# Optimization experiments

Hardware: AMD Instinct MI355X
Metric: run time of the kernel (lower is better)

## Reference

```python
import jax, jax.numpy as jnp
import numpy as np

N = 100_000      # nodes
E = 1_600_000    # edges
EL = 200_000     # labeled edge pairs
NODE_DIM, HID = 32, 256
H2, H4 = HID // 2, HID // 4  # 128, 64


def _lin(k, fan_in, fan_out):
    kw, kb = jax.random.split(k)
    bound = 1.0 / np.sqrt(fan_in)
    W = jax.random.uniform(kw, (fan_in, fan_out), jnp.float32, -bound, bound)
    b = jax.random.uniform(kb, (fan_out,), jnp.float32, -bound, bound)
    return W, b


def setup_inputs() -> dict:
    key = jax.random.key(0)
    ks = jax.random.split(key, 12)
    x = jax.random.normal(ks[0], (N, NODE_DIM), jnp.float32)
    edge_index = jax.random.randint(ks[1], (2, E), 0, N, jnp.int64)
    edge_label_index = jax.random.randint(ks[2], (2, EL), 0, N, jnp.int64)
    enc_w1, enc_b1 = _lin(ks[3], NODE_DIM, HID)
    enc_w2, enc_b2 = _lin(ks[4], HID, H2)
    conv_w0, conv_b0 = _lin(ks[5], H2, H4)
    conv_w1, conv_b1 = _lin(ks[6], H4, H4)
    conv_w2, conv_b2 = _lin(ks[7], H4, H4)
    ep_w1, ep_b1 = _lin(ks[8], 2 * H4, H2)
    ep_w2, ep_b2 = _lin(ks[9], H2, H4)
    ep_w3, ep_b3 = _lin(ks[10], H4, 1)
    return dict(x=x, edge_index=edge_index, edge_label_index=edge_label_index,
                enc_w1=enc_w1, enc_b1=enc_b1, enc_w2=enc_w2, enc_b2=enc_b2,
                conv_w0=conv_w0, conv_b0=conv_b0, conv_w1=conv_w1, conv_b1=conv_b1,
                conv_w2=conv_w2, conv_b2=conv_b2,
                ep_w1=ep_w1, ep_b1=ep_b1, ep_w2=ep_w2, ep_b2=ep_b2, ep_w3=ep_w3, ep_b3=ep_b3)


def reference(x, edge_index, edge_label_index,
              enc_w1, enc_b1, enc_w2, enc_b2,
              conv_w0, conv_b0, conv_w1, conv_b1, conv_w2, conv_b2,
              ep_w1, ep_b1, ep_w2, ep_b2, ep_w3, ep_b3):
    # node encoder (dropout = identity in eval)
    h = jax.nn.relu(x @ enc_w1 + enc_b1)
    h = jax.nn.relu(h @ enc_w2 + enc_b2)           # [N, 128]

    # GCN normalization with self-loops (PyG gcn_norm, edge_weight=1)
    loops = jnp.arange(N, dtype=edge_index.dtype)
    src = jnp.concatenate([edge_index[0], loops])   # [E+N]
    dst = jnp.concatenate([edge_index[1], loops])
    deg = jax.ops.segment_sum(jnp.ones(E + N, jnp.float32), dst, num_segments=N)
    dinv = jnp.where(deg > 0, jax.lax.rsqrt(jnp.maximum(deg, 1.0)), 0.0)
    norm = (dinv[src] * dinv[dst])[:, None]          # [E+N, 1]

    def gcn(h, W, b):
        xw = h @ W                                   # transform first (PyG)
        agg = jax.ops.segment_sum(xw[src] * norm, dst, num_segments=N)
        return agg + b

    for W, b in ((conv_w0, conv_b0), (conv_w1, conv_b1), (conv_w2, conv_b2)):
        h_new = jax.nn.relu(gcn(h, W, b))
        h = h + h_new if h.shape == h_new.shape else h_new
        # self.dropout -> identity in eval

    # edge predictor on labeled pairs
    ef = jnp.concatenate([h[edge_label_index[0]], h[edge_label_index[1]]], axis=1)  # [EL, 128]
    e = jax.nn.relu(ef @ ep_w1 + ep_b1)
    e = jax.nn.relu(e @ ep_w2 + ep_b2)
    e = jax.nn.sigmoid(e @ ep_w3 + ep_b3)
    return e.squeeze(-1)                             # [EL]
```

## Files before the change

### kernel.cpp

```cpp
#include <hip/hip_runtime.h>
#include <math.h>


#define N_NODES 100000
#define N_EDGES 1600000
#define N_EL    200000

#define KBUCK   196
#define WSHIFT  9
#define WMASK   511
#define BCAP    64
#define BSTRIDE 12288
#define PART_NB 512
#define CHUNK   3125
#define LCAP    10240
#define ENC_NB  1563

typedef __attribute__((ext_vector_type(8))) short short8_t;
typedef __attribute__((ext_vector_type(4))) float f32x4;

__device__ __forceinline__ unsigned short f2bf(float f) {
    unsigned u = __float_as_uint(f);
    unsigned r = u + 0x7FFFu + ((u >> 16) & 1u);
    return (unsigned short)(r >> 16);
}

__device__ __forceinline__ float2 up16(unsigned u) {
    union { unsigned v; _Float16 h[2]; } c; c.v = u;
    return make_float2((float)c.h[0], (float)c.h[1]);
}

template<int KTOT, int NTOT>
__device__ __forceinline__ void wprep_one(const float* __restrict__ W, unsigned short* __restrict__ Wp, int flat) {
    if (flat >= KTOT * NTOT) return;
    int j = flat & 7, lane = (flat >> 3) & 63, kstep = (flat >> 9) & 1;
    int rest = flat >> 10;
    int ntile = rest % (NTOT / 16), chunk = rest / (NTOT / 16);
    int k = chunk * 64 + kstep * 32 + (lane >> 4) * 8 + j;
    int n = ntile * 16 + (lane & 15);
    Wp[flat] = f2bf(W[(size_t)k * NTOT + n]);
}

__device__ __forceinline__ void wprep32_one(const float* __restrict__ W, unsigned short* __restrict__ Wp, int flat) {
    if (flat >= 32 * 256) return;
    int j = flat & 7, lane = (flat >> 3) & 63, ntile = flat >> 9;
    int k = (lane >> 4) * 8 + j;
    int n = ntile * 16 + (lane & 15);
    Wp[flat] = f2bf(W[(size_t)k * 256 + n]);
}

__global__ __launch_bounds__(256) void prep0(
    const float* w2, const float* w0, const float* w1, const float* wpp2, const float* w1e,
    const float* wc1, const float* wc2,
    unsigned short* p2, unsigned short* p0, unsigned short* p1, unsigned short* pp2,
    unsigned short* p1e, unsigned short* pc1, unsigned short* pc2,
    int* btail)
{
    int blk = blockIdx.x, t = threadIdx.x;
    if      (blk < 128) wprep_one<256, 128>(w2,  p2,  blk * 256 + t);
    else if (blk < 160) wprep_one<128,  64>(w0,  p0,  (blk - 128) * 256 + t);
    else if (blk < 224) wprep_one<128, 128>(w1,  p1,  (blk - 160) * 256 + t);
    else if (blk < 256) wprep_one<128,  64>(wpp2, pp2, (blk - 224) * 256 + t);
    else if (blk < 288) wprep32_one(w1e, p1e, (blk - 256) * 256 + t);
    else if (blk < 304) wprep_one< 64,  64>(wc1, pc1, (blk - 288) * 256 + t);
    else if (blk < 320) wprep_one< 64,  64>(wc2, pc2, (blk - 304) * 256 + t);
    else                btail[t] = 0;
}

__device__ __forceinline__ void fill_part_body(unsigned char* sm,
                                               const int* __restrict__ ei,
                                               int* __restrict__ btail, int* __restrict__ bscr)
{
    int (*lbuf)[BCAP] = (int(*)[BCAP])sm;
    int* lcnt  = (int*)(sm + 50176);
    int* offs  = lcnt + KBUCK;
    int* gbase = offs + KBUCK + 1;
    int t = threadIdx.x;

    for (int i = t; i < KBUCK; i += 256) lcnt[i] = 0;
    __syncthreads();

    int e0   = blockIdx.x * CHUNK;
    int eend = e0 + CHUNK; if (eend > N_EDGES) eend = N_EDGES;
    for (int e = e0 + t; e < eend; e += 256) {
        int s = __builtin_nontemporal_load(ei + e);
        int d = __builtin_nontemporal_load(ei + N_EDGES + e);
        int b = d >> WSHIFT;
        int entry = ((d & WMASK) << 17) | s;
        int pos = atomicAdd(&lcnt[b], 1);
        if (pos < BCAP) lbuf[b][pos] = entry;
        else {
            int p = atomicAdd(&btail[b], 1);
            bscr[b * BSTRIDE + p] = entry;
        }
    }
    __syncthreads();

    if (t < KBUCK) {
        int c = lcnt[t]; if (c > BCAP) c = BCAP;
        lcnt[t] = c;
        gbase[t] = atomicAdd(&btail[t], c);
    }
    __syncthreads();
    if (t == 0) {
        offs[0] = 0;
        for (int b = 0; b < KBUCK; ++b) offs[b + 1] = offs[b] + lcnt[b];
    }
    __syncthreads();

    int T = offs[KBUCK];
    for (int i = t; i < T; i += 256) {
        int loB = 0, hiB = KBUCK;
        while (hiB - loB > 1) { int mid = (loB + hiB) >> 1; if (offs[mid] <= i) loB = mid; else hiB = mid; }
        int j = i - offs[loB];
        bscr[loB * BSTRIDE + gbase[loB] + j] = lbuf[loB][j];
    }
}

__device__ __forceinline__ void encfull_body(unsigned char* sm, int bid,
    const float* __restrict__ x,
    const unsigned short* __restrict__ Wp1, const float* __restrict__ b1,
    const unsigned short* __restrict__ Wp2, const float* __restrict__ b2,
    const unsigned short* __restrict__ Wp0,
    _Float16* __restrict__ yout, int M)
{
    unsigned short* smem = (unsigned short*)sm;
    unsigned short (*As)[40]   = (unsigned short(*)[40])smem;
    unsigned short* Wls1       = smem + 2560;
    unsigned short (*H1)[264]  = (unsigned short(*)[264])smem;
    unsigned short (*H128)[136]= (unsigned short(*)[136])smem;
    unsigned short* Wls2       = smem + 16896;
    unsigned short* W0s        = smem + 16896;

    int t = threadIdx.x, wave = t >> 6, lane = t & 63;
    int m0 = bid * 64;
    int cb = lane & 15, rq = lane >> 4;

    {
        int row = t >> 2, seg = t & 3;
        int gr = m0 + row;
        float4 a = make_float4(0.f, 0.f, 0.f, 0.f), b = a;
        if (gr < M) {
            a = *(const float4*)&x[(size_t)gr * 32 + seg * 8];
            b = *(const float4*)&x[(size_t)gr * 32 + seg * 8 + 4];
        }
        unsigned short tmp[8] = { f2bf(a.x), f2bf(a.y), f2bf(a.z), f2bf(a.w),
                                  f2bf(b.x), f2bf(b.y), f2bf(b.z), f2bf(b.w) };
        *(uint4*)&As[row][seg * 8] = *(uint4*)tmp;
    }
    #pragma unroll
    for (int j = 0; j < 4; ++j)
        ((uint4*)Wls1)[t + j * 256] = ((const uint4*)Wp1)[t + j * 256];
    __syncthreads();

    short8_t af1 = *(const short8_t*)&As[wave * 16 + cb][rq * 8];
    f32x4 acc[16];
    #pragma unroll
    for (int nt = 0; nt < 16; ++nt) {
        short8_t bf = *(const short8_t*)&Wls1[(nt * 64 + lane) * 8];
        acc[nt] = __builtin_amdgcn_mfma_f32_16x16x32_bf16(af1, bf, (f32x4){0.f, 0.f, 0.f, 0.f}, 0, 0, 0);
    }
    __syncthreads();

    #pragma unroll
    for (int nt = 0; nt < 16; ++nt) {
        int col = nt * 16 + cb;
        float bv = b1[col];
        #pragma unroll
        for (int r = 0; r < 4; ++r)
            H1[wave * 16 + rq * 4 + r][col] = f2bf(fmaxf(acc[nt][r] + bv, 0.f));
    }

    f32x4 acc2[8];
    #pragma unroll
    for (int nt = 0; nt < 8; ++nt) acc2[nt] = (f32x4){0.f, 0.f, 0.f, 0.f};
    for (int ch = 0; ch < 4; ++ch) {
        #pragma unroll
        for (int j = 0; j < 4; ++j)
            ((uint4*)Wls2)[t + j * 256] = ((const uint4*)(Wp2 + (size_t)ch * 8192))[t + j * 256];
        __syncthreads();
        #pragma unroll
        for (int ks = 0; ks < 2; ++ks) {
            short8_t af = *(const short8_t*)&H1[wave * 16 + cb][ch * 64 + ks * 32 + rq * 8];
            #pragma unroll
            for (int nt = 0; nt < 8; ++nt) {
                short8_t bf = *(const short8_t*)&Wls2[((nt * 2 + ks) * 64 + lane) * 8];
                acc2[nt] = __builtin_amdgcn_mfma_f32_16x16x32_bf16(af, bf, acc2[nt], 0, 0, 0);
            }
        }
        __syncthreads();
    }

    #pragma unroll
    for (int nt = 0; nt < 8; ++nt) {
        int col = nt * 16 + cb;
        float bv = b2[col];
        #pragma unroll
        for (int r = 0; r < 4; ++r)
            H128[wave * 16 + rq * 4 + r][col] = f2bf(fmaxf(acc2[nt][r] + bv, 0.f));
    }
    ((uint4*)W0s)[t]       = ((const uint4*)Wp0)[t];
    ((uint4*)W0s)[t + 256] = ((const uint4*)Wp0)[t + 256];
    __syncthreads();

    f32x4 acc3[4];
    #pragma unroll
    for (int nt = 0; nt < 4; ++nt) acc3[nt] = (f32x4){0.f, 0.f, 0.f, 0.f};
    #pragma unroll
    for (int ch = 0; ch < 2; ++ch) {
        #pragma unroll
        for (int ks = 0; ks < 2; ++ks) {
            short8_t af = *(const short8_t*)&H128[wave * 16 + cb][ch * 64 + ks * 32 + rq * 8];
            #pragma unroll
            for (int nt = 0; nt < 4; ++nt) {
                short8_t bf = *(const short8_t*)&W0s[(((ch * 4 + nt) * 2 + ks) * 64 + lane) * 8];
                acc3[nt] = __builtin_amdgcn_mfma_f32_16x16x32_bf16(af, bf, acc3[nt], 0, 0, 0);
            }
        }
    }

    #pragma unroll
    for (int nt = 0; nt < 4; ++nt) {
        int col = nt * 16 + cb;
        #pragma unroll
        for (int r = 0; r < 4; ++r) {
            int gr = m0 + wave * 16 + rq * 4 + r;
            if (gr < M) yout[(size_t)gr * 64 + col] = (_Float16)(acc3[nt][r]);
        }
    }
}

__global__ __launch_bounds__(256, 3) void mega_fill_enc(
    const int* __restrict__ ei, int* __restrict__ btail, int* __restrict__ bscr,
    const float* __restrict__ x,
    const unsigned short* __restrict__ Wp1, const float* __restrict__ b1,
    const unsigned short* __restrict__ Wp2, const float* __restrict__ b2,
    const unsigned short* __restrict__ Wp0,
    _Float16* __restrict__ yout)
{
    __shared__ __align__(16) unsigned char sm[52544];
    if (blockIdx.x < PART_NB)
        fill_part_body(sm, ei, btail, bscr);
    else
        encfull_body(sm, blockIdx.x - PART_NB, x, Wp1, b1, Wp2, b2, Wp0, yout, N_NODES);
}

__global__ __launch_bounds__(512) void fill_place(const int* __restrict__ btail,
                                                  const int* __restrict__ bscr,
                                                  int* __restrict__ row_ptr, float* __restrict__ dinv,
                                                  int* __restrict__ col) {
    __shared__ int ssm[256];
    __shared__ int lcnt[512];
    __shared__ int lpre[512];
    __shared__ int lbuf[LCAP];
    int b = blockIdx.x, t = threadIdx.x;

    if (t < 256) ssm[t] = (t < KBUCK) ? btail[t] : 0;
    lcnt[t] = 0;
    __syncthreads();
    for (int s = 1; s < 256; s <<= 1) {
        int a = 0;
        if (t < 256 && t >= s) a = ssm[t - s];
        __syncthreads();
        if (t < 256) ssm[t] += a;
        __syncthreads();
    }
    int segstart = (b == 0) ? 0 : ssm[b - 1];
    int n = btail[b];
    const int* src = bscr + b * BSTRIDE;
    for (int i = t; i < n; i += 512)
        atomicAdd(&lcnt[src[i] >> 17], 1);
    __syncthreads();

    int c = lcnt[t];
    lpre[t] = c; __syncthreads();
    for (int s = 1; s < 512; s <<= 1) {
        int a = (t >= s) ? lpre[t - s] : 0;
        __syncthreads();
        lpre[t] += a;
        __syncthreads();
    }
    int excl = lpre[t] - c;

    int v = (b << WSHIFT) + t;
    if (v < N_NODES) {
        row_ptr[v] = segstart + excl;
        dinv[v] = rsqrtf((float)(c + 1));
    }
    if (b == KBUCK - 1 && t == 0) row_ptr[N_NODES] = N_EDGES;
    lcnt[t] = excl;
    __syncthreads();

    if (n <= LCAP) {
        for (int i = t; i < n; i += 512) {
            int e = src[i];
            int pos = atomicAdd(&lcnt[e >> 17], 1);
            lbuf[pos] = e & 0x1FFFF;
        }
        __syncthreads();
        for (int i = t; i < n; i += 512)
            col[segstart + i] = lbuf[i];
    } else {
        for (int i = t; i < n; i += 512) {
            int e = src[i];
            int pos = atomicAdd(&lcnt[e >> 17], 1);
            col[segstart + pos] = e & 0x1FFFF;
        }
    }
}

template<bool RESIDUAL, bool EDGE_DINV>
__device__ __forceinline__ void aggcv_body(
    const uint4* __restrict__ y4, const int* __restrict__ row_ptr, const int* __restrict__ col,
    const float* __restrict__ dinv, const float* __restrict__ bias,
    const unsigned short* __restrict__ Wp,
    float* __restrict__ h,
    _Float16* __restrict__ yout)
{
    __shared__ __align__(16) unsigned short Ws[4096];
    __shared__ __align__(16) unsigned short Hs[32][72];
    __shared__ float Dv[32];

    int t = threadIdx.x;
    ((uint4*)Ws)[t]       = ((const uint4*)Wp)[t];
    ((uint4*)Ws)[t + 256] = ((const uint4*)Wp)[t + 256];

    int n  = t >> 3;
    int sl = t & 7;
    int v  = blockIdx.x * 32 + n;

    float dv = dinv[v];

    float s[8];
    {
        uint4 a = y4[(size_t)v * 8 + sl];
        float2 g;
        float w = EDGE_DINV ? dv : 1.0f;
        if (EDGE_DINV) {
            g = up16(a.x); s[0] = w * g.x; s[1] = w * g.y;  g = up16(a.y); s[2] = w * g.x; s[3] = w * g.y;
            g = up16(a.z); s[4] = w * g.x; s[5] = w * g.y;  g = up16(a.w); s[6] = w * g.x; s[7] = w * g.y;
        } else {
            g = up16(a.x); s[0] = g.x; s[1] = g.y;  g = up16(a.y); s[2] = g.x; s[3] = g.y;
            g = up16(a.z); s[4] = g.x; s[5] = g.y;  g = up16(a.w); s[6] = g.x; s[7] = g.y;
        }
    }
    auto accrow = [&](uint4 f, float w) {
        float2 g;
        if (EDGE_DINV) {
            g = up16(f.x); s[0] += w * g.x; s[1] += w * g.y;  g = up16(f.y); s[2] += w * g.x; s[3] += w * g.y;
            g = up16(f.z); s[4] += w * g.x; s[5] += w * g.y;  g = up16(f.w); s[6] += w * g.x; s[7] += w * g.y;
        } else {
            g = up16(f.x); s[0] += g.x; s[1] += g.y;  g = up16(f.y); s[2] += g.x; s[3] += g.y;
            g = up16(f.z); s[4] += g.x; s[5] += g.y;  g = up16(f.w); s[6] += g.x; s[7] += g.y;
        }
    };

    int rs = row_ptr[v], re = row_ptr[v + 1];
    int i = rs;
    for (; i + 7 < re; i += 8) {
        int u0 = col[i],     u1 = col[i + 1], u2 = col[i + 2], u3 = col[i + 3];
        int u4 = col[i + 4], u5 = col[i + 5], u6 = col[i + 6], u7 = col[i + 7];
        float d0 = EDGE_DINV ? dinv[u0] : 1.0f, d1 = EDGE_DINV ? dinv[u1] : 1.0f;
        float d2 = EDGE_DINV ? dinv[u2] : 1.0f, d3 = EDGE_DINV ? dinv[u3] : 1.0f;
        float d4 = EDGE_DINV ? dinv[u4] : 1.0f, d5 = EDGE_DINV ? dinv[u5] : 1.0f;
        float d6 = EDGE_DINV ? dinv[u6] : 1.0f, d7 = EDGE_DINV ? dinv[u7] : 1.0f;
        uint4 f0 = y4[(size_t)u0 * 8 + sl];
        uint4 f1 = y4[(size_t)u1 * 8 + sl];
        uint4 f2 = y4[(size_t)u2 * 8 + sl];
        uint4 f3 = y4[(size_t)u3 * 8 + sl];
        uint4 f4 = y4[(size_t)u4 * 8 + sl];
        uint4 f5 = y4[(size_t)u5 * 8 + sl];
        uint4 f6 = y4[(size_t)u6 * 8 + sl];
        uint4 f7 = y4[(size_t)u7 * 8 + sl];
        accrow(f0, d0); accrow(f1, d1); accrow(f2, d2); accrow(f3, d3);
        accrow(f4, d4); accrow(f5, d5); accrow(f6, d6); accrow(f7, d7);
    }
    for (; i + 3 < re; i += 4) {
        int u0 = col[i], u1 = col[i + 1], u2 = col[i + 2], u3 = col[i + 3];
        float d0 = EDGE_DINV ? dinv[u0] : 1.0f, d1 = EDGE_DINV ? dinv[u1] : 1.0f;
        float d2 = EDGE_DINV ? dinv[u2] : 1.0f, d3 = EDGE_DINV ? dinv[u3] : 1.0f;
        uint4 f0 = y4[(size_t)u0 * 8 + sl];
        uint4 f1 = y4[(size_t)u1 * 8 + sl];
        uint4 f2 = y4[(size_t)u2 * 8 + sl];
        uint4 f3 = y4[(size_t)u3 * 8 + sl];
        accrow(f0, d0); accrow(f1, d1); accrow(f2, d2); accrow(f3, d3);
    }
    for (; i < re; ++i) {
        int u = col[i];
        float d = EDGE_DINV ? dinv[u] : 1.0f;
        accrow(y4[(size_t)u * 8 + sl], d);
    }

    float4 ba = *(const float4*)&bias[sl * 8];
    float4 bb = *(const float4*)&bias[sl * 8 + 4];
    float v0 = fmaxf(dv * s[0] + ba.x, 0.f), v1 = fmaxf(dv * s[1] + ba.y, 0.f);
    float v2 = fmaxf(dv * s[2] + ba.z, 0.f), v3 = fmaxf(dv * s[3] + ba.w, 0.f);
    float v4 = fmaxf(dv * s[4] + bb.x, 0.f), v5 = fmaxf(dv * s[5] + bb.y, 0.f);
    float v6 = fmaxf(dv * s[6] + bb.z, 0.f), v7 = fmaxf(dv * s[7] + bb.w, 0.f);
    if (RESIDUAL) {
        float4 h0 = *(const float4*)&h[(size_t)v * 64 + sl * 8];
        float4 h1 = *(const float4*)&h[(size_t)v * 64 + sl * 8 + 4];
        v0 += h0.x; v1 += h0.y; v2 += h0.z; v3 += h0.w;
        v4 += h1.x; v5 += h1.y; v6 += h1.z; v7 += h1.w;
    }
    *(float4*)&h[(size_t)v * 64 + sl * 8]     = make_float4(v0, v1, v2, v3);
    *(float4*)&h[(size_t)v * 64 + sl * 8 + 4] = make_float4(v4, v5, v6, v7);
    union { unsigned short us[8]; uint4 u; } hb;
    hb.us[0] = f2bf(v0); hb.us[1] = f2bf(v1); hb.us[2] = f2bf(v2); hb.us[3] = f2bf(v3);
    hb.us[4] = f2bf(v4); hb.us[5] = f2bf(v5); hb.us[6] = f2bf(v6); hb.us[7] = f2bf(v7);
    *(uint4*)&Hs[n][sl * 8] = hb.u;
    if (sl == 0) Dv[n] = dv;
    __syncthreads();

    int wave = t >> 6, lane = t & 63;
    int rt   = wave & 1;
    int ct0  = (wave >> 1) * 2;
    f32x4 acc0 = (f32x4){0.f, 0.f, 0.f, 0.f}, acc1 = acc0;
    #pragma unroll
    for (int ks = 0; ks < 2; ++ks) {
        short8_t af = *(const short8_t*)&Hs[rt * 16 + (lane & 15)][ks * 32 + (lane >> 4) * 8];
        short8_t b0 = *(const short8_t*)&Ws[((ct0 * 2 + ks) * 64 + lane) * 8];
        short8_t b1 = *(const short8_t*)&Ws[(((ct0 + 1) * 2 + ks) * 64 + lane) * 8];
        acc0 = __builtin_amdgcn_mfma_f32_16x16x32_bf16(af, b0, acc0, 0, 0, 0);
        acc1 = __builtin_amdgcn_mfma_f32_16x16x32_bf16(af, b1, acc1, 0, 0, 0);
    }
    int cb = lane & 15, rq = lane >> 4;
    #pragma unroll
    for (int r = 0; r < 4; ++r) {
        int row = rt * 16 + rq * 4 + r;
        float dv2 = Dv[row];
        size_t go = (size_t)(blockIdx.x * 32 + row) * 64;
        yout[go + ct0 * 16 + cb]       = (_Float16)(acc0[r] * dv2);
        yout[go + (ct0 + 1) * 16 + cb] = (_Float16)(acc1[r] * dv2);
    }
}

__global__ __launch_bounds__(256, 6) void aggcv0_kernel(
    const uint4* y, const int* rp, const int* col, const float* dinv, const float* b,
    const unsigned short* Wp, float* h, _Float16* yout) {
    aggcv_body<false, true>(y, rp, col, dinv, b, Wp, h, yout);
}
__global__ __launch_bounds__(256, 6) void aggcv1_kernel(
    const uint4* y, const int* rp, const int* col, const float* dinv, const float* b,
    const unsigned short* Wp, float* h, _Float16* yout) {
    aggcv_body<true, false>(y, rp, col, dinv, b, Wp, h, yout);
}

__global__ __launch_bounds__(256) void agg2_kernel(
    const uint4* __restrict__ y4, const int* __restrict__ row_ptr, const int* __restrict__ col,
    const float* __restrict__ dinv, const float* __restrict__ bias,
    const float* __restrict__ hprev, uint4* __restrict__ hb4)
{
    int v  = blockIdx.x * 32 + (threadIdx.x >> 3);
    int sl = threadIdx.x & 7;
    if (v >= N_NODES) return;

    float s[8];
    {
        uint4 a = y4[(size_t)v * 8 + sl];
        float2 g;
        g = up16(a.x); s[0] = g.x; s[1] = g.y;  g = up16(a.y); s[2] = g.x; s[3] = g.y;
        g = up16(a.z); s[4] = g.x; s[5] = g.y;  g = up16(a.w); s[6] = g.x; s[7] = g.y;
    }
    auto accrow = [&](uint4 f) {
        float2 g;
        g = up16(f.x); s[0] += g.x; s[1] += g.y;  g = up16(f.y); s[2] += g.x; s[3] += g.y;
        g = up16(f.z); s[4] += g.x; s[5] += g.y;  g = up16(f.w); s[6] += g.x; s[7] += g.y;
    };

    int rs = row_ptr[v], re = row_ptr[v + 1];
    int i = rs;
    for (; i + 7 < re; i += 8) {
        int u0 = col[i],     u1 = col[i + 1], u2 = col[i + 2], u3 = col[i + 3];
        int u4 = col[i + 4], u5 = col[i + 5], u6 = col[i + 6], u7 = col[i + 7];
        uint4 f0 = y4[(size_t)u0 * 8 + sl];
        uint4 f1 = y4[(size_t)u1 * 8 + sl];
        uint4 f2 = y4[(size_t)u2 * 8 + sl];
        uint4 f3 = y4[(size_t)u3 * 8 + sl];
        uint4 f4 = y4[(size_t)u4 * 8 + sl];
        uint4 f5 = y4[(size_t)u5 * 8 + sl];
        uint4 f6 = y4[(size_t)u6 * 8 + sl];
        uint4 f7 = y4[(size_t)u7 * 8 + sl];
        accrow(f0); accrow(f1); accrow(f2); accrow(f3);
        accrow(f4); accrow(f5); accrow(f6); accrow(f7);
    }
    for (; i + 3 < re; i += 4) {
        int u0 = col[i], u1 = col[i + 1], u2 = col[i + 2], u3 = col[i + 3];
        uint4 f0 = y4[(size_t)u0 * 8 + sl];
        uint4 f1 = y4[(size_t)u1 * 8 + sl];
        uint4 f2 = y4[(size_t)u2 * 8 + sl];
        uint4 f3 = y4[(size_t)u3 * 8 + sl];
        accrow(f0); accrow(f1); accrow(f2); accrow(f3);
    }
    for (; i < re; ++i) accrow(y4[(size_t)col[i] * 8 + sl]);

    float dv = dinv[v];
    float4 ba = *(const float4*)&bias[sl * 8];
    float4 bb = *(const float4*)&bias[sl * 8 + 4];
    float v0 = fmaxf(dv * s[0] + ba.x, 0.f), v1 = fmaxf(dv * s[1] + ba.y, 0.f);
    float v2 = fmaxf(dv * s[2] + ba.z, 0.f), v3 = fmaxf(dv * s[3] + ba.w, 0.f);
    float v4 = fmaxf(dv * s[4] + bb.x, 0.f), v5 = fmaxf(dv * s[5] + bb.y, 0.f);
    float v6 = fmaxf(dv * s[6] + bb.z, 0.f), v7 = fmaxf(dv * s[7] + bb.w, 0.f);
    {
        float4 h0 = *(const float4*)&hprev[(size_t)v * 64 + sl * 8];
        float4 h1 = *(const float4*)&hprev[(size_t)v * 64 + sl * 8 + 4];
        v0 += h0.x; v1 += h0.y; v2 += h0.z; v3 += h0.w;
        v4 += h1.x; v5 += h1.y; v6 += h1.z; v7 += h1.w;
    }
    uint4 p;
    p.x = (unsigned)f2bf(v0) | ((unsigned)f2bf(v1) << 16);
    p.y = (unsigned)f2bf(v2) | ((unsigned)f2bf(v3) << 16);
    p.z = (unsigned)f2bf(v4) | ((unsigned)f2bf(v5) << 16);
    p.w = (unsigned)f2bf(v6) | ((unsigned)f2bf(v7) << 16);
    hb4[(size_t)v * 8 + sl] = p;
}

__global__ __launch_bounds__(256, 4) void mfma_ep12(
    const unsigned short* __restrict__ A, const int* __restrict__ gidx,
    const unsigned short* __restrict__ Wp1, const float* __restrict__ b1,
    const unsigned short* __restrict__ Wp2, const float* __restrict__ b2,
    const float* __restrict__ w3, const float* __restrict__ b3,
    float* __restrict__ out, int M)
{
    __shared__ __align__(16) unsigned short smem[12800];
    unsigned short (*As)[72] = (unsigned short(*)[72])smem;
    unsigned short* Wls = smem + 4608;

    int t = threadIdx.x, wave = t >> 6, lane = t & 63;
    int m0 = blockIdx.x * 64;
    int cb = lane & 15, rq = lane >> 4;

    f32x4 acc[8];
    #pragma unroll
    for (int nt = 0; nt < 8; ++nt) acc[nt] = (f32x4){0.f, 0.f, 0.f, 0.f};

    for (int ch = 0; ch < 2; ++ch) {
        #pragma unroll
        for (int j = 0; j < 2; ++j) {
            int idx = t + j * 256;
            int row = idx >> 3, seg = idx & 7;
            int gr = m0 + row;
            uint4 v = make_uint4(0u, 0u, 0u, 0u);
            if (gr < M) {
                int node = (ch == 0) ? gidx[gr] : gidx[N_EL + gr];
                v = *(const uint4*)(A + (size_t)node * 64 + seg * 8);
            }
            *(uint4*)&As[row][seg * 8] = v;
        }
        #pragma unroll
        for (int j = 0; j < 4; ++j) {
            int idx = t + j * 256;
            ((uint4*)Wls)[idx] = ((const uint4*)(Wp1 + (size_t)ch * 8192))[idx];
        }
        __syncthreads();

        #pragma unroll
        for (int ks = 0; ks < 2; ++ks) {
            short8_t af = *(const short8_t*)&As[wave * 16 + cb][ks * 32 + rq * 8];
            #pragma unroll
            for (int nt = 0; nt < 8; ++nt) {
                short8_t bf = *(const short8_t*)&Wls[((nt * 2 + ks) * 64 + lane) * 8];
                acc[nt] = __builtin_amdgcn_mfma_f32_16x16x32_bf16(af, bf, acc[nt], 0, 0, 0);
            }
        }
        __syncthreads();
    }

    unsigned short (*E1)[136] = (unsigned short(*)[136])smem;
    unsigned short* W2s = smem + 8704;
    #pragma unroll
    for (int nt = 0; nt < 8; ++nt) {
        int col = nt * 16 + cb;
        float bv = b1[col];
        #pragma unroll
        for (int r = 0; r < 4; ++r) {
            int row = wave * 16 + rq * 4 + r;
            E1[row][col] = f2bf(fmaxf(acc[nt][r] + bv, 0.f));
        }
    }
    ((uint4*)W2s)[t]       = ((const uint4*)Wp2)[t];
    ((uint4*)W2s)[t + 256] = ((const uint4*)Wp2)[t + 256];
    __syncthreads();

    f32x4 acc2[4];
    #pragma unroll
    for (int nt = 0; nt < 4; ++nt) acc2[nt] = (f32x4){0.f, 0.f, 0.f, 0.f};
    #pragma unroll
    for (int ch = 0; ch < 2; ++ch) {
        #pragma unroll
        for (int ks = 0; ks < 2; ++ks) {
            short8_t af = *(const short8_t*)&E1[wave * 16 + cb][ch * 64 + ks * 32 + rq * 8];
            #pragma unroll
            for (int nt = 0; nt < 4; ++nt) {
                short8_t bf = *(const short8_t*)&W2s[(((ch * 4 + nt) * 2 + ks) * 64 + lane) * 8];
                acc2[nt] = __builtin_amdgcn_mfma_f32_16x16x32_bf16(af, bf, acc2[nt], 0, 0, 0);
            }
        }
    }

    float s0 = 0.f, s1 = 0.f, s2 = 0.f, s3 = 0.f;
    #pragma unroll
    for (int nt = 0; nt < 4; ++nt) {
        int col = nt * 16 + cb;
        float bv = b2[col], wv = w3[col];
        s0 += fmaxf(acc2[nt][0] + bv, 0.f) * wv;
        s1 += fmaxf(acc2[nt][1] + bv, 0.f) * wv;
        s2 += fmaxf(acc2[nt][2] + bv, 0.f) * wv;
        s3 += fmaxf(acc2[nt][3] + bv, 0.f) * wv;
    }
    #pragma unroll
    for (int off = 1; off < 16; off <<= 1) {
        s0 += __shfl_xor(s0, off);
        s1 += __shfl_xor(s1, off);
        s2 += __shfl_xor(s2, off);
        s3 += __shfl_xor(s3, off);
    }
    if (cb == 0) {
        int gr = m0 + wave * 16 + rq * 4;
        if (gr + 3 < M) {
            float bb = b3[0];
            float4 o;
            o.x = 1.f / (1.f + expf(-(s0 + bb)));
            o.y = 1.f / (1.f + expf(-(s1 + bb)));
            o.z = 1.f / (1.f + expf(-(s2 + bb)));
            o.w = 1.f / (1.f + expf(-(s3 + bb)));
            *(float4*)&out[gr] = o;
        }
    }
}

extern "C" void kernel_launch(void* const* d_in, const int* in_sizes, int n_in,
                              void* d_out, int out_size, void* d_ws, size_t ws_size,
                              hipStream_t stream) {
    const float* x       = (const float*)d_in[0];
    const int*   ei      = (const int*)d_in[1];
    const int*   eli     = (const int*)d_in[2];
    const float* enc_w1  = (const float*)d_in[3];
    const float* enc_b1  = (const float*)d_in[4];
    const float* enc_w2  = (const float*)d_in[5];
    const float* enc_b2  = (const float*)d_in[6];
    const float* conv_w0 = (const float*)d_in[7];
    const float* conv_b0 = (const float*)d_in[8];
    const float* conv_w1 = (const float*)d_in[9];
    const float* conv_b1 = (const float*)d_in[10];
    const float* conv_w2 = (const float*)d_in[11];
    const float* conv_b2 = (const float*)d_in[12];
    const float* ep_w1   = (const float*)d_in[13];
    const float* ep_b1   = (const float*)d_in[14];
    const float* ep_w2   = (const float*)d_in[15];
    const float* ep_b2   = (const float*)d_in[16];
    const float* ep_w3   = (const float*)d_in[17];
    const float* ep_b3   = (const float*)d_in[18];
    float* out = (float*)d_out;

    float* fws = (float*)d_ws;
    _Float16* yb         = (_Float16*)fws;
    float* h64           = fws + 3200000;
    unsigned short* h64b = (unsigned short*)(fws + 9600000);
    int*   col     = (int*)(fws + 12800000);
    int*   row_ptr = col + 1600000;
    float* dinvp   = (float*)(row_ptr + 100032);
    unsigned short* w2p = (unsigned short*)(dinvp + 100000);
    unsigned short* w0p = w2p + 32768;
    unsigned short* w1p = w0p + 8192;
    unsigned short* wp2 = w1p + 16384;
    unsigned short* w1e = wp2 + 8192;
    unsigned short* wc1p = w1e + 8192;
    unsigned short* wc2p = wc1p + 4096;
    int*   btail   = (int*)(wc2p + 4096);
    int*   bscr    = btail + 256;

    _Float16* yb2 = (_Float16*)h64b;

    const int GBE = N_EL / 64;
    const int GBA = N_NODES / 32;

    prep0<<<321, 256, 0, stream>>>(enc_w2, conv_w0, ep_w1, ep_w2, enc_w1, conv_w1, conv_w2,
                                   w2p, w0p, w1p, wp2, w1e, wc1p, wc2p, btail);

    mega_fill_enc<<<PART_NB + ENC_NB, 256, 0, stream>>>(ei, btail, bscr,
        x, w1e, enc_b1, w2p, enc_b2, w0p, yb);

    fill_place<<<KBUCK, 512, 0, stream>>>(btail, bscr, row_ptr, dinvp, col);

    aggcv0_kernel<<<GBA, 256, 0, stream>>>((const uint4*)yb, row_ptr, col, dinvp, conv_b0,
                                           wc1p, h64, yb2);
    aggcv1_kernel<<<GBA, 256, 0, stream>>>((const uint4*)yb2, row_ptr, col, dinvp, conv_b1,
                                           wc2p, h64, yb);
    agg2_kernel<<<GBA, 256, 0, stream>>>((const uint4*)yb, row_ptr, col, dinvp, conv_b2,
                                         h64, (uint4*)h64b);

    mfma_ep12<<<GBE, 256, 0, stream>>>(h64b, eli, w1p, ep_b1, wp2, ep_b2, ep_w3, ep_b3, out, N_EL);
}
```

Measured before the change: 280.9 us.

## Defer weight prep into fill_place, parallel scan offsets, nontemporal col/h accesses

```diff
diff --git a/kernel.cpp b/kernel.cpp
--- a/kernel.cpp
+++ b/kernel.cpp
@@ -15,9 +15,11 @@
 #define CHUNK   3125
 #define LCAP    10240
 #define ENC_NB  1563
+#define PLACE_XB 64
 
 typedef __attribute__((ext_vector_type(8))) short short8_t;
 typedef __attribute__((ext_vector_type(4))) float f32x4;
+typedef __attribute__((ext_vector_type(4))) float f32x4v;
 
 __device__ __forceinline__ unsigned short f2bf(float f) {
     unsigned u = __float_as_uint(f);
@@ -50,20 +52,14 @@
 }
 
 __global__ __launch_bounds__(256) void prep0(
-    const float* w2, const float* w0, const float* w1, const float* wpp2, const float* w1e,
-    const float* wc1, const float* wc2,
-    unsigned short* p2, unsigned short* p0, unsigned short* p1, unsigned short* pp2,
-    unsigned short* p1e, unsigned short* pc1, unsigned short* pc2,
+    const float* w2, const float* w0, const float* w1e,
+    unsigned short* p2, unsigned short* p0, unsigned short* p1e,
     int* btail)
 {
     int blk = blockIdx.x, t = threadIdx.x;
     if      (blk < 128) wprep_one<256, 128>(w2,  p2,  blk * 256 + t);
     else if (blk < 160) wprep_one<128,  64>(w0,  p0,  (blk - 128) * 256 + t);
-    else if (blk < 224) wprep_one<128, 128>(w1,  p1,  (blk - 160) * 256 + t);
-    else if (blk < 256) wprep_one<128,  64>(wpp2, pp2, (blk - 224) * 256 + t);
-    else if (blk < 288) wprep32_one(w1e, p1e, (blk - 256) * 256 + t);
-    else if (blk < 304) wprep_one< 64,  64>(wc1, pc1, (blk - 288) * 256 + t);
-    else if (blk < 320) wprep_one< 64,  64>(wc2, pc2, (blk - 304) * 256 + t);
+    else if (blk < 192) wprep32_one(w1e, p1e, (blk - 160) * 256 + t);
     else                btail[t] = 0;
 }
 
@@ -71,10 +67,12 @@
                                                const int* __restrict__ ei,
                                                int* __restrict__ btail, int* __restrict__ bscr)
 {
-    int (*lbuf)[BCAP] = (int(*)[BCAP])sm;
-    int* lcnt  = (int*)(sm + 50176);
-    int* offs  = lcnt + KBUCK;
-    int* gbase = offs + KBUCK + 1;
+    int* base = (int*)sm;
+    int (*lbuf)[BCAP] = (int(*)[BCAP])base;
+    int* lcnt  = base + 12544;
+    int* offs  = base + 12740;
+    int* gbase = base + 12937;
+    int* sscan = base + 13133;
     int t = threadIdx.x;
 
     for (int i = t; i < KBUCK; i += 256) lcnt[i] = 0;
@@ -91,21 +89,27 @@
         if (pos < BCAP) lbuf[b][pos] = entry;
         else {
             int p = atomicAdd(&btail[b], 1);
-            bscr[b * BSTRIDE + p] = entry;
-        }
-    }
-    __syncthreads();
-
+            __builtin_nontemporal_store(entry, bscr + b * BSTRIDE + p);
+        }
+    }
+    __syncthreads();
+
+    int myc = 0;
     if (t < KBUCK) {
-        int c = lcnt[t]; if (c > BCAP) c = BCAP;
-        lcnt[t] = c;
-        gbase[t] = atomicAdd(&btail[t], c);
-    }
-    __syncthreads();
-    if (t == 0) {
-        offs[0] = 0;
-        for (int b = 0; b < KBUCK; ++b) offs[b + 1] = offs[b] + lcnt[b];
-    }
+        myc = lcnt[t]; if (myc > BCAP) myc = BCAP;
+        lcnt[t] = myc;
+        gbase[t] = atomicAdd(&btail[t], myc);
+    }
+    sscan[t] = (t < KBUCK) ? myc : 0;
+    __syncthreads();
+    for (int s = 1; s < 256; s <<= 1) {
+        int a = (t >= s) ? sscan[t - s] : 0;
+        __syncthreads();
+        sscan[t] += a;
+        __syncthreads();
+    }
+    if (t < KBUCK) offs[t + 1] = sscan[t];
+    if (t == 0) offs[0] = 0;
     __syncthreads();
 
     int T = offs[KBUCK];
@@ -113,7 +117,7 @@
         int loB = 0, hiB = KBUCK;
         while (hiB - loB > 1) { int mid = (loB + hiB) >> 1; if (offs[mid] <= i) loB = mid; else hiB = mid; }
         int j = i - offs[loB];
-        bscr[loB * BSTRIDE + gbase[loB] + j] = lbuf[loB][j];
+        __builtin_nontemporal_store(lbuf[loB][j], bscr + loB * BSTRIDE + gbase[loB] + j);
     }
 }
 
@@ -238,7 +242,7 @@
     const unsigned short* __restrict__ Wp0,
     _Float16* __restrict__ yout)
 {
-    __shared__ __align__(16) unsigned char sm[52544];
+    __shared__ __align__(16) unsigned char sm[53568];
     if (blockIdx.x < PART_NB)
         fill_part_body(sm, ei, btail, bscr);
     else
@@ -248,12 +252,24 @@
 __global__ __launch_bounds__(512) void fill_place(const int* __restrict__ btail,
                                                   const int* __restrict__ bscr,
                                                   int* __restrict__ row_ptr, float* __restrict__ dinv,
-                                                  int* __restrict__ col) {
+                                                  int* __restrict__ col,
+    const float* w1, const float* wpp2, const float* wc1, const float* wc2,
+    unsigned short* p1, unsigned short* pp2, unsigned short* pc1, unsigned short* pc2)
+{
     __shared__ int ssm[256];
     __shared__ int lcnt[512];
     __shared__ int lpre[512];
     __shared__ int lbuf[LCAP];
     int b = blockIdx.x, t = threadIdx.x;
+
+    if (b >= KBUCK) {
+        int blk = b - KBUCK;
+        if      (blk < 32) wprep_one<128, 128>(w1,  p1,  blk * 512 + t);
+        else if (blk < 48) wprep_one<128,  64>(wpp2, pp2, (blk - 32) * 512 + t);
+        else if (blk < 56) wprep_one< 64,  64>(wc1, pc1, (blk - 48) * 512 + t);
+        else               wprep_one< 64,  64>(wc2, pc2, (blk - 56) * 512 + t);
+        return;
+    }
 
     if (t < 256) ssm[t] = (t < KBUCK) ? btail[t] : 0;
     lcnt[t] = 0;
@@ -358,8 +374,14 @@
     int rs = row_ptr[v], re = row_ptr[v + 1];
     int i = rs;
     for (; i + 7 < re; i += 8) {
-        int u0 = col[i],     u1 = col[i + 1], u2 = col[i + 2], u3 = col[i + 3];
-        int u4 = col[i + 4], u5 = col[i + 5], u6 = col[i + 6], u7 = col[i + 7];
+        int u0 = __builtin_nontemporal_load(col + i);
+        int u1 = __builtin_nontemporal_load(col + i + 1);
+        int u2 = __builtin_nontemporal_load(col + i + 2);
+        int u3 = __builtin_nontemporal_load(col + i + 3);
+        int u4 = __builtin_nontemporal_load(col + i + 4);
+        int u5 = __builtin_nontemporal_load(col + i + 5);
+        int u6 = __builtin_nontemporal_load(col + i + 6);
+        int u7 = __builtin_nontemporal_load(col + i + 7);
         float d0 = EDGE_DINV ? dinv[u0] : 1.0f, d1 = EDGE_DINV ? dinv[u1] : 1.0f;
         float d2 = EDGE_DINV ? dinv[u2] : 1.0f, d3 = EDGE_DINV ? dinv[u3] : 1.0f;
         float d4 = EDGE_DINV ? dinv[u4] : 1.0f, d5 = EDGE_DINV ? dinv[u5] : 1.0f;
@@ -376,7 +398,10 @@
         accrow(f4, d4); accrow(f5, d5); accrow(f6, d6); accrow(f7, d7);
     }
     for (; i + 3 < re; i += 4) {
-        int u0 = col[i], u1 = col[i + 1], u2 = col[i + 2], u3 = col[i + 3];
+        int u0 = __builtin_nontemporal_load(col + i);
+        int u1 = __builtin_nontemporal_load(col + i + 1);
+        int u2 = __builtin_nontemporal_load(col + i + 2);
+        int u3 = __builtin_nontemporal_load(col + i + 3);
         float d0 = EDGE_DINV ? dinv[u0] : 1.0f, d1 = EDGE_DINV ? dinv[u1] : 1.0f;
         float d2 = EDGE_DINV ? dinv[u2] : 1.0f, d3 = EDGE_DINV ? dinv[u3] : 1.0f;
         uint4 f0 = y4[(size_t)u0 * 8 + sl];
@@ -386,7 +411,7 @@
         accrow(f0, d0); accrow(f1, d1); accrow(f2, d2); accrow(f3, d3);
     }
     for (; i < re; ++i) {
-        int u = col[i];
+        int u = __builtin_nontemporal_load(col + i);
         float d = EDGE_DINV ? dinv[u] : 1.0f;
         accrow(y4[(size_t)u * 8 + sl], d);
     }
@@ -398,10 +423,10 @@
     float v4 = fmaxf(dv * s[4] + bb.x, 0.f), v5 = fmaxf(dv * s[5] + bb.y, 0.f);
     float v6 = fmaxf(dv * s[6] + bb.z, 0.f), v7 = fmaxf(dv * s[7] + bb.w, 0.f);
     if (RESIDUAL) {
-        float4 h0 = *(const float4*)&h[(size_t)v * 64 + sl * 8];
-        float4 h1 = *(const float4*)&h[(size_t)v * 64 + sl * 8 + 4];
-        v0 += h0.x; v1 += h0.y; v2 += h0.z; v3 += h0.w;
-        v4 += h1.x; v5 += h1.y; v6 += h1.z; v7 += h1.w;
+        f32x4v h0 = __builtin_nontemporal_load((const f32x4v*)&h[(size_t)v * 64 + sl * 8]);
+        f32x4v h1 = __builtin_nontemporal_load((const f32x4v*)&h[(size_t)v * 64 + sl * 8 + 4]);
+        v0 += h0[0]; v1 += h0[1]; v2 += h0[2]; v3 += h0[3];
+        v4 += h1[0]; v5 += h1[1]; v6 += h1[2]; v7 += h1[3];
     }
     *(float4*)&h[(size_t)v * 64 + sl * 8]     = make_float4(v0, v1, v2, v3);
     *(float4*)&h[(size_t)v * 64 + sl * 8 + 4] = make_float4(v4, v5, v6, v7);
@@ -471,8 +496,14 @@
     int rs = row_ptr[v], re = row_ptr[v + 1];
     int i = rs;
     for (; i + 7 < re; i += 8) {
-        int u0 = col[i],     u1 = col[i + 1], u2 = col[i + 2], u3 = col[i + 3];
-        int u4 = col[i + 4], u5 = col[i + 5], u6 = col[i + 6], u7 = col[i + 7];
+        int u0 = __builtin_nontemporal_load(col + i);
+        int u1 = __builtin_nontemporal_load(col + i + 1);
+        int u2 = __builtin_nontemporal_load(col + i + 2);
+        int u3 = __builtin_nontemporal_load(col + i + 3);
+        int u4 = __builtin_nontemporal_load(col + i + 4);
+        int u5 = __builtin_nontemporal_load(col + i + 5);
+        int u6 = __builtin_nontemporal_load(col + i + 6);
+        int u7 = __builtin_nontemporal_load(col + i + 7);
         uint4 f0 = y4[(size_t)u0 * 8 + sl];
         uint4 f1 = y4[(size_t)u1 * 8 + sl];
         uint4 f2 = y4[(size_t)u2 * 8 + sl];
@@ -485,14 +516,17 @@
         accrow(f4); accrow(f5); accrow(f6); accrow(f7);
     }
     for (; i + 3 < re; i += 4) {
-        int u0 = col[i], u1 = col[i + 1], u2 = col[i + 2], u3 = col[i + 3];
+        int u0 = __builtin_nontemporal_load(col + i);
+        int u1 = __builtin_nontemporal_load(col + i + 1);
+        int u2 = __builtin_nontemporal_load(col + i + 2);
+        int u3 = __builtin_nontemporal_load(col + i + 3);
         uint4 f0 = y4[(size_t)u0 * 8 + sl];
         uint4 f1 = y4[(size_t)u1 * 8 + sl];
         uint4 f2 = y4[(size_t)u2 * 8 + sl];
         uint4 f3 = y4[(size_t)u3 * 8 + sl];
         accrow(f0); accrow(f1); accrow(f2); accrow(f3);
     }
-    for (; i < re; ++i) accrow(y4[(size_t)col[i] * 8 + sl]);
+    for (; i < re; ++i) accrow(y4[(size_t)__builtin_nontemporal_load(col + i) * 8 + sl]);
 
     float dv = dinv[v];
     float4 ba = *(const float4*)&bias[sl * 8];
@@ -502,10 +536,10 @@
     float v4 = fmaxf(dv * s[4] + bb.x, 0.f), v5 = fmaxf(dv * s[5] + bb.y, 0.f);
     float v6 = fmaxf(dv * s[6] + bb.z, 0.f), v7 = fmaxf(dv * s[7] + bb.w, 0.f);
     {
-        float4 h0 = *(const float4*)&hprev[(size_t)v * 64 + sl * 8];
-        float4 h1 = *(const float4*)&hprev[(size_t)v * 64 + sl * 8 + 4];
-        v0 += h0.x; v1 += h0.y; v2 += h0.z; v3 += h0.w;
-        v4 += h1.x; v5 += h1.y; v6 += h1.z; v7 += h1.w;
+        f32x4v h0 = __builtin_nontemporal_load((const f32x4v*)&hprev[(size_t)v * 64 + sl * 8]);
+        f32x4v h1 = __builtin_nontemporal_load((const f32x4v*)&hprev[(size_t)v * 64 + sl * 8 + 4]);
+        v0 += h0[0]; v1 += h0[1]; v2 += h0[2]; v3 += h0[3];
+        v4 += h1[0]; v5 += h1[1]; v6 += h1[2]; v7 += h1[3];
     }
     uint4 p;
     p.x = (unsigned)f2bf(v0) | ((unsigned)f2bf(v1) << 16);
@@ -675,13 +709,13 @@
     const int GBE = N_EL / 64;
     const int GBA = N_NODES / 32;
 
-    prep0<<<321, 256, 0, stream>>>(enc_w2, conv_w0, ep_w1, ep_w2, enc_w1, conv_w1, conv_w2,
-                                   w2p, w0p, w1p, wp2, w1e, wc1p, wc2p, btail);
+    prep0<<<193, 256, 0, stream>>>(enc_w2, conv_w0, enc_w1, w2p, w0p, w1e, btail);
 
     mega_fill_enc<<<PART_NB + ENC_NB, 256, 0, stream>>>(ei, btail, bscr,
         x, w1e, enc_b1, w2p, enc_b2, w0p, yb);
 
-    fill_place<<<KBUCK, 512, 0, stream>>>(btail, bscr, row_ptr, dinvp, col);
+    fill_place<<<KBUCK + PLACE_XB, 512, 0, stream>>>(btail, bscr, row_ptr, dinvp, col,
+        ep_w1, ep_w2, conv_w1, conv_w2, w1p, wp2, wc1p, wc2p);
 
     aggcv0_kernel<<<GBA, 256, 0, stream>>>((const uint4*)yb, row_ptr, col, dinvp, conv_b0,
                                            wc1p, h64, yb2);
```

Measured after the change: 297.7 us. +6.0%, slower.

## Fuse CSR placement with node encoder and split partition into its own kernel

Applied to the files above, without the earlier changes.

```diff
diff --git a/kernel.cpp b/kernel.cpp
--- a/kernel.cpp
+++ b/kernel.cpp
@@ -71,10 +71,12 @@
                                                const int* __restrict__ ei,
                                                int* __restrict__ btail, int* __restrict__ bscr)
 {
-    int (*lbuf)[BCAP] = (int(*)[BCAP])sm;
-    int* lcnt  = (int*)(sm + 50176);
-    int* offs  = lcnt + KBUCK;
-    int* gbase = offs + KBUCK + 1;
+    int* base = (int*)sm;
+    int (*lbuf)[BCAP] = (int(*)[BCAP])base;
+    int* lcnt  = base + 12544;
+    int* offs  = base + 12740;
+    int* gbase = base + 12937;
+    int* sscan = base + 13133;
     int t = threadIdx.x;
 
     for (int i = t; i < KBUCK; i += 256) lcnt[i] = 0;
@@ -96,16 +98,22 @@
     }
     __syncthreads();
 
+    int myc = 0;
     if (t < KBUCK) {
-        int c = lcnt[t]; if (c > BCAP) c = BCAP;
-        lcnt[t] = c;
-        gbase[t] = atomicAdd(&btail[t], c);
-    }
-    __syncthreads();
-    if (t == 0) {
-        offs[0] = 0;
-        for (int b = 0; b < KBUCK; ++b) offs[b + 1] = offs[b] + lcnt[b];
-    }
+        myc = lcnt[t]; if (myc > BCAP) myc = BCAP;
+        lcnt[t] = myc;
+        gbase[t] = atomicAdd(&btail[t], myc);
+    }
+    sscan[t] = (t < KBUCK) ? myc : 0;
+    __syncthreads();
+    for (int s = 1; s < 256; s <<= 1) {
+        int a = (t >= s) ? sscan[t - s] : 0;
+        __syncthreads();
+        sscan[t] += a;
+        __syncthreads();
+    }
+    if (t < KBUCK) offs[t + 1] = sscan[t];
+    if (t == 0) offs[0] = 0;
     __syncthreads();
 
     int T = offs[KBUCK];
@@ -114,6 +122,78 @@
         while (hiB - loB > 1) { int mid = (loB + hiB) >> 1; if (offs[mid] <= i) loB = mid; else hiB = mid; }
         int j = i - offs[loB];
         bscr[loB * BSTRIDE + gbase[loB] + j] = lbuf[loB][j];
+    }
+}
+
+__global__ __launch_bounds__(256) void fill_part(const int* __restrict__ ei,
+                                                 int* __restrict__ btail, int* __restrict__ bscr)
+{
+    __shared__ __align__(16) unsigned char sm[53568];
+    fill_part_body(sm, ei, btail, bscr);
+}
+
+__device__ __forceinline__ void fill_place_body(unsigned char* sm, int b,
+    const int* __restrict__ btail, const int* __restrict__ bscr,
+    int* __restrict__ row_ptr, float* __restrict__ dinv, int* __restrict__ col)
+{
+    int* base = (int*)sm;
+    int* ssm  = base;
+    int* lcnt = base + 256;
+    int* lpre = base + 768;
+    int* lbuf = base + 1280;
+    int t = threadIdx.x;
+
+    if (t < 256) ssm[t] = (t < KBUCK) ? btail[t] : 0;
+    lcnt[t] = 0;
+    __syncthreads();
+    for (int s = 1; s < 256; s <<= 1) {
+        int a = 0;
+        if (t < 256 && t >= s) a = ssm[t - s];
+        __syncthreads();
+        if (t < 256) ssm[t] += a;
+        __syncthreads();
+    }
+    int segstart = (b == 0) ? 0 : ssm[b - 1];
+    int n = btail[b];
+    const int* src = bscr + b * BSTRIDE;
+    for (int i = t; i < n; i += 512)
+        atomicAdd(&lcnt[src[i] >> 17], 1);
+    __syncthreads();
+
+    int c = lcnt[t];
+    lpre[t] = c; __syncthreads();
+    for (int s = 1; s < 512; s <<= 1) {
+        int a = (t >= s) ? lpre[t - s] : 0;
+        __syncthreads();
+        lpre[t] += a;
+        __syncthreads();
+    }
+    int excl = lpre[t] - c;
+
+    int v = (b << WSHIFT) + t;
+    if (v < N_NODES) {
+        row_ptr[v] = segstart + excl;
+        dinv[v] = rsqrtf((float)(c + 1));
+    }
+    if (b == KBUCK - 1 && t == 0) row_ptr[N_NODES] = N_EDGES;
+    lcnt[t] = excl;
+    __syncthreads();
+
+    if (n <= LCAP) {
+        for (int i = t; i < n; i += 512) {
+            int e = src[i];
+            int pos = atomicAdd(&lcnt[e >> 17], 1);
+            lbuf[pos] = e & 0x1FFFF;
+        }
+        __syncthreads();
+        for (int i = t; i < n; i += 512)
+            col[segstart + i] = lbuf[i];
+    } else {
+        for (int i = t; i < n; i += 512) {
+            int e = src[i];
+            int pos = atomicAdd(&lcnt[e >> 17], 1);
+            col[segstart + pos] = e & 0x1FFFF;
+        }
     }
 }
 
@@ -132,43 +212,44 @@
     unsigned short* Wls2       = smem + 16896;
     unsigned short* W0s        = smem + 16896;
 
-    int t = threadIdx.x, wave = t >> 6, lane = t & 63;
+    int t = threadIdx.x;
+    int wave = t >> 6, lane = t & 63;
     int m0 = bid * 64;
     int cb = lane & 15, rq = lane >> 4;
 
     {
-        int row = t >> 2, seg = t & 3;
+        int row = t >> 3, seg = t & 7;
         int gr = m0 + row;
-        float4 a = make_float4(0.f, 0.f, 0.f, 0.f), b = a;
-        if (gr < M) {
-            a = *(const float4*)&x[(size_t)gr * 32 + seg * 8];
-            b = *(const float4*)&x[(size_t)gr * 32 + seg * 8 + 4];
-        }
-        unsigned short tmp[8] = { f2bf(a.x), f2bf(a.y), f2bf(a.z), f2bf(a.w),
-                                  f2bf(b.x), f2bf(b.y), f2bf(b.z), f2bf(b.w) };
-        *(uint4*)&As[row][seg * 8] = *(uint4*)tmp;
-    }
-    #pragma unroll
-    for (int j = 0; j < 4; ++j)
-        ((uint4*)Wls1)[t + j * 256] = ((const uint4*)Wp1)[t + j * 256];
-    __syncthreads();
-
-    short8_t af1 = *(const short8_t*)&As[wave * 16 + cb][rq * 8];
+        float4 a = make_float4(0.f, 0.f, 0.f, 0.f);
+        if (gr < M) a = *(const float4*)&x[(size_t)gr * 32 + seg * 4];
+        unsigned short tmp[4] = { f2bf(a.x), f2bf(a.y), f2bf(a.z), f2bf(a.w) };
+        *(uint2*)&As[row][seg * 4] = *(uint2*)tmp;
+    }
+    #pragma unroll
+    for (int j = 0; j < 2; ++j)
+        ((uint4*)Wls1)[t + j * 512] = ((const uint4*)Wp1)[t + j * 512];
+    __syncthreads();
+
     f32x4 acc[16];
-    #pragma unroll
-    for (int nt = 0; nt < 16; ++nt) {
-        short8_t bf = *(const short8_t*)&Wls1[(nt * 64 + lane) * 8];
-        acc[nt] = __builtin_amdgcn_mfma_f32_16x16x32_bf16(af1, bf, (f32x4){0.f, 0.f, 0.f, 0.f}, 0, 0, 0);
-    }
-    __syncthreads();
-
-    #pragma unroll
-    for (int nt = 0; nt < 16; ++nt) {
-        int col = nt * 16 + cb;
-        float bv = b1[col];
-        #pragma unroll
-        for (int r = 0; r < 4; ++r)
-            H1[wave * 16 + rq * 4 + r][col] = f2bf(fmaxf(acc[nt][r] + bv, 0.f));
+    if (wave < 4) {
+        short8_t af1 = *(const short8_t*)&As[wave * 16 + cb][rq * 8];
+        #pragma unroll
+        for (int nt = 0; nt < 16; ++nt) {
+            short8_t bf = *(const short8_t*)&Wls1[(nt * 64 + lane) * 8];
+            acc[nt] = __builtin_amdgcn_mfma_f32_16x16x32_bf16(af1, bf, (f32x4){0.f, 0.f, 0.f, 0.f}, 0, 0, 0);
+        }
+    }
+    __syncthreads();
+
+    if (wave < 4) {
+        #pragma unroll
+        for (int nt = 0; nt < 16; ++nt) {
+            int col = nt * 16 + cb;
+            float bv = b1[col];
+            #pragma unroll
+            for (int r = 0; r < 4; ++r)
+                H1[wave * 16 + rq * 4 + r][col] = f2bf(fmaxf(acc[nt][r] + bv, 0.f));
+        }
     }
 
     f32x4 acc2[8];
@@ -176,137 +257,78 @@
     for (int nt = 0; nt < 8; ++nt) acc2[nt] = (f32x4){0.f, 0.f, 0.f, 0.f};
     for (int ch = 0; ch < 4; ++ch) {
         #pragma unroll
-        for (int j = 0; j < 4; ++j)
-            ((uint4*)Wls2)[t + j * 256] = ((const uint4*)(Wp2 + (size_t)ch * 8192))[t + j * 256];
-        __syncthreads();
-        #pragma unroll
-        for (int ks = 0; ks < 2; ++ks) {
-            short8_t af = *(const short8_t*)&H1[wave * 16 + cb][ch * 64 + ks * 32 + rq * 8];
+        for (int j = 0; j < 2; ++j)
+            ((uint4*)Wls2)[t + j * 512] = ((const uint4*)(Wp2 + (size_t)ch * 8192))[t + j * 512];
+        __syncthreads();
+        if (wave < 4) {
             #pragma unroll
-            for (int nt = 0; nt < 8; ++nt) {
-                short8_t bf = *(const short8_t*)&Wls2[((nt * 2 + ks) * 64 + lane) * 8];
-                acc2[nt] = __builtin_amdgcn_mfma_f32_16x16x32_bf16(af, bf, acc2[nt], 0, 0, 0);
+            for (int ks = 0; ks < 2; ++ks) {
+                short8_t af = *(const short8_t*)&H1[wave * 16 + cb][ch * 64 + ks * 32 + rq * 8];
+                #pragma unroll
+                for (int nt = 0; nt < 8; ++nt) {
+                    short8_t bf = *(const short8_t*)&Wls2[((nt * 2 + ks) * 64 + lane) * 8];
+                    acc2[nt] = __builtin_amdgcn_mfma_f32_16x16x32_bf16(af, bf, acc2[nt], 0, 0, 0);
+                }
             }
         }
         __syncthreads();
     }
 
-    #pragma unroll
-    for (int nt = 0; nt < 8; ++nt) {
-        int col = nt * 16 + cb;
-        float bv = b2[col];
-        #pragma unroll
-        for (int r = 0; r < 4; ++r)
-            H128[wave * 16 + rq * 4 + r][col] = f2bf(fmaxf(acc2[nt][r] + bv, 0.f));
-    }
-    ((uint4*)W0s)[t]       = ((const uint4*)Wp0)[t];
-    ((uint4*)W0s)[t + 256] = ((const uint4*)Wp0)[t + 256];
-    __syncthreads();
-
-    f32x4 acc3[4];
-    #pragma unroll
-    for (int nt = 0; nt < 4; ++nt) acc3[nt] = (f32x4){0.f, 0.f, 0.f, 0.f};
-    #pragma unroll
-    for (int ch = 0; ch < 2; ++ch) {
-        #pragma unroll
-        for (int ks = 0; ks < 2; ++ks) {
-            short8_t af = *(const short8_t*)&H128[wave * 16 + cb][ch * 64 + ks * 32 + rq * 8];
+    if (wave < 4) {
+        #pragma unroll
+        for (int nt = 0; nt < 8; ++nt) {
+            int col = nt * 16 + cb;
+            float bv = b2[col];
             #pragma unroll
-            for (int nt = 0; nt < 4; ++nt) {
-                short8_t bf = *(const short8_t*)&W0s[(((ch * 4 + nt) * 2 + ks) * 64 + lane) * 8];
-                acc3[nt] = __builtin_amdgcn_mfma_f32_16x16x32_bf16(af, bf, acc3[nt], 0, 0, 0);
+            for (int r = 0; r < 4; ++r)
+                H128[wave * 16 + rq * 4 + r][col] = f2bf(fmaxf(acc2[nt][r] + bv, 0.f));
+        }
+    }
+    ((uint4*)W0s)[t] = ((const uint4*)Wp0)[t];
+    __syncthreads();
+
+    if (wave < 4) {
+        f32x4 acc3[4];
+        #pragma unroll
+        for (int nt = 0; nt < 4; ++nt) acc3[nt] = (f32x4){0.f, 0.f, 0.f, 0.f};
+        #pragma unroll
+        for (int ch = 0; ch < 2; ++ch) {
+            #pragma unroll
+            for (int ks = 0; ks < 2; ++ks) {
+                short8_t af = *(const short8_t*)&H128[wave * 16 + cb][ch * 64 + ks * 32 + rq * 8];
+                #pragma unroll
+                for (int nt = 0; nt < 4; ++nt) {
+                    short8_t bf = *(const short8_t*)&W0s[(((ch * 4 + nt) * 2 + ks) * 64 + lane) * 8];
+                    acc3[nt] = __builtin_amdgcn_mfma_f32_16x16x32_bf16(af, bf, acc3[nt], 0, 0, 0);
+                }
             }
         }
-    }
-
-    #pragma unroll
-    for (int nt = 0; nt < 4; ++nt) {
-        int col = nt * 16 + cb;
-        #pragma unroll
-        for (int r = 0; r < 4; ++r) {
-            int gr = m0 + wave * 16 + rq * 4 + r;
-            if (gr < M) yout[(size_t)gr * 64 + col] = (_Float16)(acc3[nt][r]);
-        }
-    }
-}
-
-__global__ __launch_bounds__(256, 3) void mega_fill_enc(
-    const int* __restrict__ ei, int* __restrict__ btail, int* __restrict__ bscr,
+        #pragma unroll
+        for (int nt = 0; nt < 4; ++nt) {
+            int col = nt * 16 + cb;
+            #pragma unroll
+            for (int r = 0; r < 4; ++r) {
+                int gr = m0 + wave * 16 + rq * 4 + r;
+                if (gr < M) yout[(size_t)gr * 64 + col] = (_Float16)(acc3[nt][r]);
+            }
+        }
+    }
+}
+
+__global__ __launch_bounds__(512, 6) void mega_place_enc(
+    const int* __restrict__ btail, const int* __restrict__ bscr,
+    int* __restrict__ row_ptr, float* __restrict__ dinv, int* __restrict__ col,
     const float* __restrict__ x,
     const unsigned short* __restrict__ Wp1, const float* __restrict__ b1,
     const unsigned short* __restrict__ Wp2, const float* __restrict__ b2,
     const unsigned short* __restrict__ Wp0,
     _Float16* __restrict__ yout)
 {
-    __shared__ __align__(16) unsigned char sm[52544];
-    if (blockIdx.x < PART_NB)
-        fill_part_body(sm, ei, btail, bscr);
+    __shared__ __align__(16) unsigned char sm[50176];
+    if (blockIdx.x < KBUCK)
+        fill_place_body(sm, blockIdx.x, btail, bscr, row_ptr, dinv, col);
     else
-        encfull_body(sm, blockIdx.x - PART_NB, x, Wp1, b1, Wp2, b2, Wp0, yout, N_NODES);
-}
-
-__global__ __launch_bounds__(512) void fill_place(const int* __restrict__ btail,
-                                                  const int* __restrict__ bscr,
-                                                  int* __restrict__ row_ptr, float* __restrict__ dinv,
-                                                  int* __restrict__ col) {
-    __shared__ int ssm[256];
-    __shared__ int lcnt[512];
-    __shared__ int lpre[512];
-    __shared__ int lbuf[LCAP];
-    int b = blockIdx.x, t = threadIdx.x;
-
-    if (t < 256) ssm[t] = (t < KBUCK) ? btail[t] : 0;
-    lcnt[t] = 0;
-    __syncthreads();
-    for (int s = 1; s < 256; s <<= 1) {
-        int a = 0;
-        if (t < 256 && t >= s) a = ssm[t - s];
-        __syncthreads();
-        if (t < 256) ssm[t] += a;
-        __syncthreads();
-    }
-    int segstart = (b == 0) ? 0 : ssm[b - 1];
-    int n = btail[b];
-    const int* src = bscr + b * BSTRIDE;
-    for (int i = t; i < n; i += 512)
-        atomicAdd(&lcnt[src[i] >> 17], 1);
-    __syncthreads();
-
-    int c = lcnt[t];
-    lpre[t] = c; __syncthreads();
-    for (int s = 1; s < 512; s <<= 1) {
-        int a = (t >= s) ? lpre[t - s] : 0;
-        __syncthreads();
-        lpre[t] += a;
-        __syncthreads();
-    }
-    int excl = lpre[t] - c;
-
-    int v = (b << WSHIFT) + t;
-    if (v < N_NODES) {
-        row_ptr[v] = segstart + excl;
-        dinv[v] = rsqrtf((float)(c + 1));
-    }
-    if (b == KBUCK - 1 && t == 0) row_ptr[N_NODES] = N_EDGES;
-    lcnt[t] = excl;
-    __syncthreads();
-
-    if (n <= LCAP) {
-        for (int i = t; i < n; i += 512) {
-            int e = src[i];
-            int pos = atomicAdd(&lcnt[e >> 17], 1);
-            lbuf[pos] = e & 0x1FFFF;
-        }
-        __syncthreads();
-        for (int i = t; i < n; i += 512)
-            col[segstart + i] = lbuf[i];
-    } else {
-        for (int i = t; i < n; i += 512) {
-            int e = src[i];
-            int pos = atomicAdd(&lcnt[e >> 17], 1);
-            col[segstart + pos] = e & 0x1FFFF;
-        }
-    }
+        encfull_body(sm, blockIdx.x - KBUCK, x, Wp1, b1, Wp2, b2, Wp0, yout, N_NODES);
 }
 
 template<bool RESIDUAL, bool EDGE_DINV>
@@ -678,10 +700,10 @@
     prep0<<<321, 256, 0, stream>>>(enc_w2, conv_w0, ep_w1, ep_w2, enc_w1, conv_w1, conv_w2,
                                    w2p, w0p, w1p, wp2, w1e, wc1p, wc2p, btail);
 
-    mega_fill_enc<<<PART_NB + ENC_NB, 256, 0, stream>>>(ei, btail, bscr,
+    fill_part<<<PART_NB, 256, 0, stream>>>(ei, btail, bscr);
+
+    mega_place_enc<<<KBUCK + ENC_NB, 512, 0, stream>>>(btail, bscr, row_ptr, dinvp, col,
         x, w1e, enc_b1, w2p, enc_b2, w0p, yb);
-
-    fill_place<<<KBUCK, 512, 0, stream>>>(btail, bscr, row_ptr, dinvp, col);
 
     aggcv0_kernel<<<GBA, 256, 0, stream>>>((const uint4*)yb, row_ptr, col, dinvp, conv_b0,
                                            wc1p, h64, yb2);
```

Result: no change. 284.5 us (+1.3%).
